# Kernel tuning notes

Measured on AMD Instinct MI355X. Metric: run time of the kernel, lower is better.

## Reference

```python
import jax, jax.numpy as jnp
import numpy as np

C = 256
NUM_HEADS = 4
REDUCTION = 4
RED = C // REDUCTION           # 64
HEAD_DIM = RED // NUM_HEADS    # 16
SCALE = HEAD_DIM ** -0.5
LN_EPS = 1e-5


def setup_inputs() -> dict:
    key = jax.random.key(0)
    ks = jax.random.split(key, 9)
    B, H, W = 2, 64, 64
    x = jax.random.normal(ks[0], (B, C, H, W), dtype=jnp.float32)
    # LayerNorm params
    norm_w = jnp.ones((C,), jnp.float32)
    norm_b = jnp.zeros((C,), jnp.float32)
    # Linear weights (torch layout: [out, in]), y = x @ W.T
    qkv_w = jax.random.normal(ks[1], (3 * RED, C), jnp.float32) * (C ** -0.5)
    out_w = jax.random.normal(ks[2], (C, RED), jnp.float32) * (RED ** -0.5)
    # 1x1 conv weights, stored as [out_c, in_c]
    conv1_w = jax.random.normal(ks[3], (C // 2, C), jnp.float32) * (C ** -0.5)
    conv1_b = jax.random.normal(ks[4], (C // 2,), jnp.float32) * 0.01
    conv2_w = jax.random.normal(ks[5], (1, C // 2), jnp.float32) * ((C // 2) ** -0.5)
    conv2_b = jax.random.normal(ks[6], (1,), jnp.float32) * 0.01
    gamma = jnp.ones((1,), jnp.float32) * 0.5  # nonzero so output depends on attention
    return {"x": x, "norm_w": norm_w, "norm_b": norm_b, "qkv_w": qkv_w,
            "out_w": out_w, "conv1_w": conv1_w, "conv1_b": conv1_b,
            "conv2_w": conv2_w, "conv2_b": conv2_b, "gamma": gamma}


def reference(x, norm_w, norm_b, qkv_w, out_w, conv1_w, conv1_b, conv2_w, conv2_b, gamma):
    B, C_, H, W = x.shape
    N = H * W
    # [B, N, C]
    xf = x.reshape(B, C_, N).transpose(0, 2, 1)
    # LayerNorm over channel dim
    mu = jnp.mean(xf, axis=-1, keepdims=True)
    var = jnp.mean(jnp.square(xf - mu), axis=-1, keepdims=True)
    xn = (xf - mu) * jax.lax.rsqrt(var + LN_EPS) * norm_w + norm_b
    # QKV projection -> [B, N, 3*RED]
    qkv = jnp.einsum('bnc,oc->bno', xn, qkv_w)
    q, k, v = jnp.split(qkv, 3, axis=-1)
    def heads(t):  # [B, N, RED] -> [B, h, N, d]
        return t.reshape(B, N, NUM_HEADS, HEAD_DIM).transpose(0, 2, 1, 3)
    q, k, v = heads(q), heads(k), heads(v)
    attn = jax.nn.softmax(jnp.einsum('bhnd,bhmd->bhnm', q, k) * SCALE, axis=-1)
    # dynamic weight branch: two 1x1 convs on raw x
    d1 = jax.nn.relu(jnp.einsum('oc,bchw->bohw', conv1_w, x) + conv1_b[None, :, None, None])
    dyn = (jnp.einsum('oc,bchw->bohw', conv2_w, d1) + conv2_b[None, :, None, None])  # [B,1,H,W]
    dyn = dyn.reshape(B, 1, N)  # broadcast over heads
    # per-query row scaling of attention
    attn = attn * dyn[:, :, :, None]
    out = jnp.einsum('bhnm,bhmd->bhnd', attn, v)            # [B,h,N,d]
    out = out.transpose(0, 2, 1, 3).reshape(B, N, RED)      # [B,N,RED]
    out = jnp.einsum('bnr,cr->bnc', out, out_w)             # [B,N,C]
    out = out.transpose(0, 2, 1).reshape(B, C_, H, W)
    return jax.nn.sigmoid(gamma[0] * out + x)
```

## Files before the change

kernel.cpp:

```cpp
#include <hip/hip_runtime.h>
#include <cstdint>
#include <cstddef>

#define LOG2E 1.44269504088896340736f

typedef float  f32x16 __attribute__((ext_vector_type(16)));
typedef __bf16 bf16x8 __attribute__((ext_vector_type(8)));

union BF8 { bf16x8 v; uint u[4]; ushort us[8]; };

__device__ __forceinline__ uint pack_bf(float a, float b) {
    uint ua = __float_as_uint(a) + 0x8000u;
    uint ub = __float_as_uint(b) + 0x8000u;
    return __builtin_amdgcn_perm(ub, ua, 0x07060302u);
}
__device__ __forceinline__ float bf_lo(uint u) { return __uint_as_float(u << 16); }
__device__ __forceinline__ float bf_hi(uint u) { return __uint_as_float(u & 0xFFFF0000u); }

__global__ __launch_bounds__(256) void convert_w_kernel(
    const float* __restrict__ qkv_w, const float* __restrict__ c1w,
    const float* __restrict__ out_w,
    ushort* __restrict__ qkvw_b, ushort* __restrict__ c1w_b, ushort* __restrict__ ow_b)
{
    const int g = (blockIdx.x * 256 + threadIdx.x) * 4;
    const float* src; ushort* dst; int off; float sc = 1.f;
    if (g < 49152)      { src = qkv_w; dst = qkvw_b; off = g;
                          if (g < 16384) sc = 0.25f * LOG2E; }
    else if (g < 81920) { src = c1w;   dst = c1w_b;  off = g - 49152; }
    else                { src = out_w; dst = ow_b;   off = g - 81920; }
    float4 v = *(const float4*)(src + off);
    uint2 pk;
    pk.x = pack_bf(v.x * sc, v.y * sc);
    pk.y = pack_bf(v.z * sc, v.w * sc);
    *(uint2*)(dst + off) = pk;
}

__global__ __launch_bounds__(256) void lnqkv_kernel(
    const float* __restrict__ x, const float* __restrict__ nw, const float* __restrict__ nb,
    const ushort* __restrict__ qkvw_b, const ushort* __restrict__ c1w_b,
    const float* __restrict__ c1b, const float* __restrict__ c2w,
    const float* __restrict__ c2b,
    ushort* __restrict__ Qb, ushort* __restrict__ Kb, ushort* __restrict__ Vsw,
    float* __restrict__ dynb)
{
    __shared__ uint  XN[32 * 32 * 4];
    __shared__ uint  XR[32 * 32 * 4];
    __shared__ float trans[4][32 * 33];
    __shared__ float red1[256], red2[256];
    __shared__ float muS[32], rsS[32];

    const int t    = threadIdx.x;
    const int pg   = blockIdx.x;
    const int b    = pg >> 7;
    const int n0   = (pg & 127) * 32;

    {
        const int j  = t & 31;
        const int cg = t >> 5;
        const size_t xb = (size_t)b * 256 * 4096 + n0 + j;
        float v[32];
        #pragma unroll
        for (int i = 0; i < 32; ++i) v[i] = x[xb + (size_t)(cg * 32 + i) * 4096];
        float s1 = 0.f, s2 = 0.f;
        #pragma unroll
        for (int i = 0; i < 32; ++i) { s1 += v[i]; s2 += v[i] * v[i]; }
        #pragma unroll
        for (int kk = 0; kk < 4; ++kk) {
            uint4 pk;
            pk.x = pack_bf(v[kk * 8 + 0], v[kk * 8 + 1]);
            pk.y = pack_bf(v[kk * 8 + 2], v[kk * 8 + 3]);
            pk.z = pack_bf(v[kk * 8 + 4], v[kk * 8 + 5]);
            pk.w = pack_bf(v[kk * 8 + 6], v[kk * 8 + 7]);
            *(uint4*)&XR[((cg * 4 + kk) * 32 + j) * 4] = pk;
        }
        red1[t] = s1; red2[t] = s2;
        __syncthreads();
        if (t < 32) {
            float a = 0.f, q = 0.f;
            #pragma unroll
            for (int g2 = 0; g2 < 8; ++g2) { a += red1[g2 * 32 + t]; q += red2[g2 * 32 + t]; }
            float mu  = a * (1.f / 256.f);
            float var = q * (1.f / 256.f) - mu * mu;
            muS[t] = mu; rsS[t] = rsqrtf(fmaxf(var, 0.f) + 1e-5f);
        }
        __syncthreads();
        const float mu = muS[j], rs = rsS[j];
        #pragma unroll
        for (int kk = 0; kk < 4; ++kk) {
            const float4 w0 = *(const float4*)(nw + cg * 32 + kk * 8);
            const float4 w1 = *(const float4*)(nw + cg * 32 + kk * 8 + 4);
            const float4 b0 = *(const float4*)(nb + cg * 32 + kk * 8);
            const float4 b1 = *(const float4*)(nb + cg * 32 + kk * 8 + 4);
            float e0 = (v[kk * 8 + 0] - mu) * rs * w0.x + b0.x;
            float e1 = (v[kk * 8 + 1] - mu) * rs * w0.y + b0.y;
            float e2 = (v[kk * 8 + 2] - mu) * rs * w0.z + b0.z;
            float e3 = (v[kk * 8 + 3] - mu) * rs * w0.w + b0.w;
            float e4 = (v[kk * 8 + 4] - mu) * rs * w1.x + b1.x;
            float e5 = (v[kk * 8 + 5] - mu) * rs * w1.y + b1.y;
            float e6 = (v[kk * 8 + 6] - mu) * rs * w1.z + b1.z;
            float e7 = (v[kk * 8 + 7] - mu) * rs * w1.w + b1.w;
            uint4 o;
            o.x = pack_bf(e0, e1); o.y = pack_bf(e2, e3);
            o.z = pack_bf(e4, e5); o.w = pack_bf(e6, e7);
            *(uint4*)&XN[((cg * 4 + kk) * 32 + j) * 4] = o;
        }
    }
    __syncthreads();

    const int w    = t >> 6;
    const int lane = t & 63;
    const int m    = lane & 31;
    const int h    = lane >> 5;
    float* tr = trans[w];
    const ushort* xnB = (const ushort*)XN;
    const ushort* xrB = (const ushort*)XR;

    if (w < 3) {
        const ushort* ap0 = qkvw_b + ((size_t)(w * 64 + m)) * 256 + h * 8;
        const ushort* ap1 = ap0 + 32 * 256;
        f32x16 acc0, acc1;
        #pragma unroll
        for (int i = 0; i < 16; ++i) { acc0[i] = 0.f; acc1[i] = 0.f; }
        #pragma unroll 4
        for (int ks = 0; ks < 16; ++ks) {
            bf16x8 bf = *(const bf16x8*)(xnB + ((ks * 2 + h) * 32 + m) * 8);
            bf16x8 a0 = *(const bf16x8*)(ap0 + ks * 16);
            bf16x8 a1 = *(const bf16x8*)(ap1 + ks * 16);
            acc0 = __builtin_amdgcn_mfma_f32_32x32x16_bf16(a0, bf, acc0, 0, 0, 0);
            acc1 = __builtin_amdgcn_mfma_f32_32x32x16_bf16(a1, bf, acc1, 0, 0, 0);
        }
        for (int ti = 0; ti < 2; ++ti) {
            const f32x16& A = ti ? acc1 : acc0;
            #pragma unroll
            for (int r = 0; r < 16; ++r)
                tr[((r & 3) + 8 * (r >> 2) + 4 * h) * 33 + m] = A[r];
            if (w < 2) {
                ushort* dst = (w == 0) ? Qb : Kb;
                #pragma unroll
                for (int it = 0; it < 2; ++it) {
                    int unit = it * 2 + h;
                    int hl = unit >> 1, half = unit & 1;
                    float v0 = tr[(hl * 16 + half * 8 + 0) * 33 + m];
                    float v1 = tr[(hl * 16 + half * 8 + 1) * 33 + m];
                    float v2 = tr[(hl * 16 + half * 8 + 2) * 33 + m];
                    float v3 = tr[(hl * 16 + half * 8 + 3) * 33 + m];
                    float v4 = tr[(hl * 16 + half * 8 + 4) * 33 + m];
                    float v5 = tr[(hl * 16 + half * 8 + 5) * 33 + m];
                    float v6 = tr[(hl * 16 + half * 8 + 6) * 33 + m];
                    float v7 = tr[(hl * 16 + half * 8 + 7) * 33 + m];
                    uint4 pk;
                    pk.x = pack_bf(v0, v1); pk.y = pack_bf(v2, v3);
                    pk.z = pack_bf(v4, v5); pk.w = pack_bf(v6, v7);
                    int head = ti * 2 + hl;
                    *(uint4*)(dst + ((size_t)(b * 4 + head) * 4096 + n0 + m) * 16 + half * 8) = pk;
                }
            } else {
                int d = lane & 15, u = lane >> 4;
                #pragma unroll
                for (int it = 0; it < 4; ++it) {
                    int unit = it * 4 + u;
                    int hl = unit >> 3, sg = unit & 7;
                    float v0 = tr[(hl * 16 + d) * 33 + sg * 4 + 0];
                    float v1 = tr[(hl * 16 + d) * 33 + sg * 4 + 1];
                    float v2 = tr[(hl * 16 + d) * 33 + sg * 4 + 2];
                    float v3 = tr[(hl * 16 + d) * 33 + sg * 4 + 3];
                    uint2 pk; pk.x = pack_bf(v0, v1); pk.y = pack_bf(v2, v3);
                    int head = ti * 2 + hl;
                    *(uint2*)(Vsw + (((size_t)(b * 4 + head) * 1024 + (pg & 127) * 8 + sg) * 16 + d) * 4) = pk;
                }
            }
        }
    } else {
        f32x16 acc[4];
        #pragma unroll
        for (int ti = 0; ti < 4; ++ti)
            #pragma unroll
            for (int i = 0; i < 16; ++i) acc[ti][i] = 0.f;
        #pragma unroll 2
        for (int ks = 0; ks < 16; ++ks) {
            bf16x8 bf = *(const bf16x8*)(xrB + ((ks * 2 + h) * 32 + m) * 8);
            #pragma unroll
            for (int ti = 0; ti < 4; ++ti) {
                bf16x8 a = *(const bf16x8*)(c1w_b + ((size_t)(ti * 32 + m)) * 256 + ks * 16 + h * 8);
                acc[ti] = __builtin_amdgcn_mfma_f32_32x32x16_bf16(a, bf, acc[ti], 0, 0, 0);
            }
        }
        float partial = 0.f;
        for (int ti = 0; ti < 4; ++ti) {
            #pragma unroll
            for (int r = 0; r < 16; ++r)
                tr[((r & 3) + 8 * (r >> 2) + 4 * h) * 33 + m] = acc[ti][r];
            #pragma unroll
            for (int i = 0; i < 16; ++i) {
                int og = ti * 32 + h * 16 + i;
                partial += fmaxf(tr[(h * 16 + i) * 33 + m] + c1b[og], 0.f) * c2w[og];
            }
        }
        float tot = partial + __shfl_xor(partial, 32);
        if (lane < 32) dynb[(size_t)b * 4096 + n0 + m] = c2b[0] + tot;
    }
}

__global__ __launch_bounds__(512) void attn_final_kernel(
    const ushort* __restrict__ Qb, const ushort* __restrict__ Kb,
    const ushort* __restrict__ Vsw, const float* __restrict__ dynb,
    const ushort* __restrict__ ow_b, const float* __restrict__ x,
    const float* __restrict__ gamma, float* __restrict__ out)
{
    __shared__ float OM[2][4][16][32];
    __shared__ float LM[2][4][32];
    __shared__ float trans[8][32 * 33];

    const int t    = threadIdx.x;
    const int w    = t >> 6;
    const int lane = t & 63;
    const int c    = lane & 31;
    const int h    = lane >> 5;
    const int hd   = w & 3;
    const int kb   = w >> 2;
    const int pg   = blockIdx.x;
    const int b    = pg >> 7;
    const int n0   = (pg & 127) * 32;
    const int bh   = b * 4 + hd;

    const bf16x8 qf = *(const bf16x8*)(Qb + ((size_t)bh * 4096 + n0 + c) * 16 + h * 8);

    f32x16 oacc, zf;
    #pragma unroll
    for (int i = 0; i < 16; ++i) { oacc[i] = 0.f; zf[i] = 0.f; }

    const ushort* kp = Kb + ((size_t)bh * 4096 + kb * 2048 + c) * 16 + h * 8;
    const ushort* vb = Vsw + (size_t)bh * 65536 + ((size_t)kb * 512 + h) * 64 + c * 4;

    #pragma unroll 2
    for (int ch = 0; ch < 64; ++ch) {
        const bf16x8 kf = *(const bf16x8*)kp;
        f32x16 s = __builtin_amdgcn_mfma_f32_32x32x16_bf16(kf, qf, zf, 0, 0, 0);

        BF8 p1, p2;
        #pragma unroll
        for (int jj = 0; jj < 4; ++jj) {
            p1.u[jj] = pack_bf(__builtin_amdgcn_exp2f(s[2*jj]),   __builtin_amdgcn_exp2f(s[2*jj+1]));
            p2.u[jj] = pack_bf(__builtin_amdgcn_exp2f(s[8+2*jj]), __builtin_amdgcn_exp2f(s[8+2*jj+1]));
        }

        BF8 a1, a2;
        if (c < 16) {
            const uint2 g1 = *(const uint2*)(vb);
            const uint2 g2 = *(const uint2*)(vb + 128);
            const uint2 g3 = *(const uint2*)(vb + 256);
            const uint2 g4 = *(const uint2*)(vb + 384);
            a1.u[0] = g1.x; a1.u[1] = g1.y; a1.u[2] = g2.x; a1.u[3] = g2.y;
            a2.u[0] = g3.x; a2.u[1] = g3.y; a2.u[2] = g4.x; a2.u[3] = g4.y;
        } else {
            const uint f = (c == 16) ? 0x3F803F80u : 0u;
            a1.u[0] = a1.u[1] = a1.u[2] = a1.u[3] = f;
            a2.u[0] = a2.u[1] = a2.u[2] = a2.u[3] = f;
        }

        oacc = __builtin_amdgcn_mfma_f32_32x32x16_bf16(a1.v, p1.v, oacc, 0, 0, 0);
        oacc = __builtin_amdgcn_mfma_f32_32x32x16_bf16(a2.v, p2.v, oacc, 0, 0, 0);

        kp += 512; vb += 512;
    }

    #pragma unroll
    for (int r = 0; r < 8; ++r)
        OM[kb][hd][(r & 3) + 8 * (r >> 2) + 4 * h][c] = oacc[r];
    if (h == 0) LM[kb][hd][c] = oacc[8];
    __syncthreads();

    const int m = c;
    const float dyn_px = dynb[(size_t)b * 4096 + n0 + m];

    f32x16 acc;
    #pragma unroll
    for (int i = 0; i < 16; ++i) acc[i] = 0.f;

    #pragma unroll
    for (int ks = 0; ks < 4; ++ks) {
        float l   = LM[0][ks][m] + LM[1][ks][m];
        float fac = dyn_px / l;
        BF8 bfr;
        #pragma unroll
        for (int i = 0; i < 4; ++i) {
            int d0 = h * 8 + 2 * i;
            float e0 = (OM[0][ks][d0][m]     + OM[1][ks][d0][m])     * fac;
            float e1 = (OM[0][ks][d0 + 1][m] + OM[1][ks][d0 + 1][m]) * fac;
            bfr.u[i] = pack_bf(e0, e1);
        }
        bf16x8 af = *(const bf16x8*)(ow_b + (size_t)(w * 32 + m) * 64 + ks * 16 + h * 8);
        acc = __builtin_amdgcn_mfma_f32_32x32x16_bf16(af, bfr.v, acc, 0, 0, 0);
    }

    float* tr = trans[w];
    const float g = gamma[0];
    #pragma unroll
    for (int r = 0; r < 16; ++r)
        tr[((r & 3) + 8 * (r >> 2) + 4 * h) * 33 + m] = acc[r];
    #pragma unroll 4
    for (int it = 0; it < 16; ++it) {
        int o = it * 2 + h;
        float vv = tr[o * 33 + m];
        size_t idx = ((size_t)b * 256 + w * 32 + o) * 4096 + n0 + m;
        float z = g * vv + x[idx];
        out[idx] = 1.f / (1.f + __builtin_amdgcn_exp2f(-z * LOG2E));
    }
}

extern "C" void kernel_launch(void* const* d_in, const int* in_sizes, int n_in,
                              void* d_out, int out_size, void* d_ws, size_t ws_size,
                              hipStream_t stream)
{
    const float* x      = (const float*)d_in[0];
    const float* norm_w = (const float*)d_in[1];
    const float* norm_b = (const float*)d_in[2];
    const float* qkv_w  = (const float*)d_in[3];
    const float* out_w  = (const float*)d_in[4];
    const float* c1w    = (const float*)d_in[5];
    const float* c1b    = (const float*)d_in[6];
    const float* c2w    = (const float*)d_in[7];
    const float* c2b    = (const float*)d_in[8];
    const float* gamma  = (const float*)d_in[9];

    char* ws = (char*)d_ws;
    ushort* Qb     = (ushort*)ws;
    ushort* Kb     = Qb + 524288;
    ushort* Vsw    = Kb + 524288;
    ushort* qkvw_b = Vsw + 524288;
    ushort* c1w_b  = qkvw_b + 49152;
    ushort* ow_b   = c1w_b + 32768;
    float*  dynb   = (float*)(ws + 3342336);

    hipLaunchKernelGGL(convert_w_kernel, dim3(96), dim3(256), 0, stream,
                       qkv_w, c1w, out_w, qkvw_b, c1w_b, ow_b);
    hipLaunchKernelGGL(lnqkv_kernel, dim3(256), dim3(256), 0, stream,
                       x, norm_w, norm_b, qkvw_b, c1w_b, c1b, c2w, c2b,
                       Qb, Kb, Vsw, dynb);
    hipLaunchKernelGGL(attn_final_kernel, dim3(256), dim3(512), 0, stream,
                       Qb, Kb, Vsw, dynb, ow_b, x, gamma, (float*)d_out);
}
```

Before: 125.2 us.

## Split attention key range across four wave groups with 1024-thread blocks

Doubles the attention block to 1024 threads so each head's key range is split four ways instead of two, halving the per-wave loop length. Partial O and L accumulators are stored as float2 in shared memory and summed across the four splits before the output projection. The epilogue now writes results straight from MFMA registers instead of transposing through shared memory. This adds more waves per block, which raises parallelism in the latency-bound softmax/PV loop, while half the waves sit idle during the epilogue and register pressure limits may tighten under the larger launch bound.

Result: faster. 114.5 us (-8.6%).

```diff
diff --git a/kernel.cpp b/kernel.cpp
--- a/kernel.cpp
+++ b/kernel.cpp
@@ -201,15 +201,14 @@
     }
 }
 
-__global__ __launch_bounds__(512) void attn_final_kernel(
+__global__ __launch_bounds__(1024) void attn_final_kernel(
     const ushort* __restrict__ Qb, const ushort* __restrict__ Kb,
     const ushort* __restrict__ Vsw, const float* __restrict__ dynb,
     const ushort* __restrict__ ow_b, const float* __restrict__ x,
     const float* __restrict__ gamma, float* __restrict__ out)
 {
-    __shared__ float OM[2][4][16][32];
-    __shared__ float LM[2][4][32];
-    __shared__ float trans[8][32 * 33];
+    __shared__ float2 OM[4][4][8][32];
+    __shared__ float  LM[4][4][32];
 
     const int t    = threadIdx.x;
     const int w    = t >> 6;
@@ -229,11 +228,11 @@
     #pragma unroll
     for (int i = 0; i < 16; ++i) { oacc[i] = 0.f; zf[i] = 0.f; }
 
-    const ushort* kp = Kb + ((size_t)bh * 4096 + kb * 2048 + c) * 16 + h * 8;
-    const ushort* vb = Vsw + (size_t)bh * 65536 + ((size_t)kb * 512 + h) * 64 + c * 4;
+    const ushort* kp = Kb + ((size_t)bh * 4096 + kb * 1024 + c) * 16 + h * 8;
+    const ushort* vb = Vsw + (size_t)bh * 65536 + ((size_t)kb * 256 + h) * 64 + c * 4;
 
     #pragma unroll 2
-    for (int ch = 0; ch < 64; ++ch) {
+    for (int ch = 0; ch < 32; ++ch) {
         const bf16x8 kf = *(const bf16x8*)kp;
         f32x16 s = __builtin_amdgcn_mfma_f32_32x32x16_bf16(kf, qf, zf, 0, 0, 0);
 
@@ -264,47 +263,49 @@
         kp += 512; vb += 512;
     }
 
-    #pragma unroll
-    for (int r = 0; r < 8; ++r)
-        OM[kb][hd][(r & 3) + 8 * (r >> 2) + 4 * h][c] = oacc[r];
+    OM[kb][hd][2 * h + 0][c] = make_float2(oacc[0], oacc[1]);
+    OM[kb][hd][2 * h + 1][c] = make_float2(oacc[2], oacc[3]);
+    OM[kb][hd][4 + 2 * h][c] = make_float2(oacc[4], oacc[5]);
+    OM[kb][hd][5 + 2 * h][c] = make_float2(oacc[6], oacc[7]);
     if (h == 0) LM[kb][hd][c] = oacc[8];
     __syncthreads();
 
-    const int m = c;
-    const float dyn_px = dynb[(size_t)b * 4096 + n0 + m];
-
-    f32x16 acc;
-    #pragma unroll
-    for (int i = 0; i < 16; ++i) acc[i] = 0.f;
-
-    #pragma unroll
-    for (int ks = 0; ks < 4; ++ks) {
-        float l   = LM[0][ks][m] + LM[1][ks][m];
-        float fac = dyn_px / l;
-        BF8 bfr;
-        #pragma unroll
-        for (int i = 0; i < 4; ++i) {
-            int d0 = h * 8 + 2 * i;
-            float e0 = (OM[0][ks][d0][m]     + OM[1][ks][d0][m])     * fac;
-            float e1 = (OM[0][ks][d0 + 1][m] + OM[1][ks][d0 + 1][m]) * fac;
-            bfr.u[i] = pack_bf(e0, e1);
-        }
-        bf16x8 af = *(const bf16x8*)(ow_b + (size_t)(w * 32 + m) * 64 + ks * 16 + h * 8);
-        acc = __builtin_amdgcn_mfma_f32_32x32x16_bf16(af, bfr.v, acc, 0, 0, 0);
-    }
-
-    float* tr = trans[w];
-    const float g = gamma[0];
-    #pragma unroll
-    for (int r = 0; r < 16; ++r)
-        tr[((r & 3) + 8 * (r >> 2) + 4 * h) * 33 + m] = acc[r];
-    #pragma unroll 4
-    for (int it = 0; it < 16; ++it) {
-        int o = it * 2 + h;
-        float vv = tr[o * 33 + m];
-        size_t idx = ((size_t)b * 256 + w * 32 + o) * 4096 + n0 + m;
-        float z = g * vv + x[idx];
-        out[idx] = 1.f / (1.f + __builtin_amdgcn_exp2f(-z * LOG2E));
+    if (w < 8) {
+        const int m = c;
+        const float dyn_px = dynb[(size_t)b * 4096 + n0 + m];
+
+        f32x16 acc;
+        #pragma unroll
+        for (int i = 0; i < 16; ++i) acc[i] = 0.f;
+
+        #pragma unroll
+        for (int ks = 0; ks < 4; ++ks) {
+            float l = LM[0][ks][m] + LM[1][ks][m] + LM[2][ks][m] + LM[3][ks][m];
+            float fac = dyn_px / l;
+            BF8 bfr;
+            #pragma unroll
+            for (int i = 0; i < 4; ++i) {
+                int sl = 4 * h + i;
+                float2 s0 = OM[0][ks][sl][m];
+                float2 s1 = OM[1][ks][sl][m];
+                float2 s2 = OM[2][ks][sl][m];
+                float2 s3 = OM[3][ks][sl][m];
+                float e0 = (s0.x + s1.x + s2.x + s3.x) * fac;
+                float e1 = (s0.y + s1.y + s2.y + s3.y) * fac;
+                bfr.u[i] = pack_bf(e0, e1);
+            }
+            bf16x8 af = *(const bf16x8*)(ow_b + (size_t)(w * 32 + m) * 64 + ks * 16 + h * 8);
+            acc = __builtin_amdgcn_mfma_f32_32x32x16_bf16(af, bfr.v, acc, 0, 0, 0);
+        }
+
+        const float g = gamma[0];
+        #pragma unroll
+        for (int r = 0; r < 16; ++r) {
+            int o = (r & 3) + 8 * (r >> 2) + 4 * h;
+            size_t idx = ((size_t)b * 256 + w * 32 + o) * 4096 + n0 + m;
+            float z = g * acc[r] + x[idx];
+            out[idx] = 1.f / (1.f + __builtin_amdgcn_exp2f(-z * LOG2E));
+        }
     }
 }
 
@@ -337,6 +338,6 @@
     hipLaunchKernelGGL(lnqkv_kernel, dim3(256), dim3(256), 0, stream,
                        x, norm_w, norm_b, qkvw_b, c1w_b, c1b, c2w, c2b,
                        Qb, Kb, Vsw, dynb);
-    hipLaunchKernelGGL(attn_final_kernel, dim3(256), dim3(512), 0, stream,
+    hipLaunchKernelGGL(attn_final_kernel, dim3(256), dim3(1024), 0, stream,
                        Qb, Kb, Vsw, dynb, ow_b, x, gamma, (float*)d_out);
 }
```
